# Performance work log

Measured on AMD Instinct MI355X. Metric: run time of the kernel, lower is better.

The kernel has to match this reference:

```python
import jax, jax.numpy as jnp
import numpy as np

B, T, C, E, KB, V = 2, 2048, 128, 16, 32, 50257
EPS = 1e-5


def layernorm(x, g, b):
    mu = jnp.mean(x, axis=-1, keepdims=True)
    var = jnp.mean((x - mu) ** 2, axis=-1, keepdims=True)
    return (x - mu) * jax.lax.rsqrt(var + EPS) * g + b


def setup_inputs() -> dict:
    key = jax.random.key(0)
    ks = jax.random.split(key, 16)
    s = 0.02
    return {
        "input_ids": jax.random.randint(ks[0], (B, T), 0, V),
        "emb": jax.random.normal(ks[1], (V, C), jnp.float32) * s,
        "router": jax.random.normal(ks[2], (E, C), jnp.float32) * s,
        "k_experts": jax.random.normal(ks[3], (E, KB, C), jnp.float32),
        "v_experts": jax.random.normal(ks[4], (E, KB, C), jnp.float32),
        "static_k": jax.random.normal(ks[5], (1, 1, KB, C), jnp.float32),
        "static_v": jax.random.normal(ks[6], (1, 1, KB, C), jnp.float32),
        "kv_gate": jnp.float32(0.0),
        "Wq": jax.random.normal(ks[7], (C, C), jnp.float32) * s,
        "Wo": jax.random.normal(ks[8], (C, C), jnp.float32) * s,
        "Wmlp": jax.random.normal(ks[9], (C, C), jnp.float32) * s,
        "bmlp": jnp.zeros((C,), jnp.float32),
        "ln1_g": jnp.ones((C,), jnp.float32),
        "ln1_b": jnp.zeros((C,), jnp.float32),
        "ln2_g": jnp.ones((C,), jnp.float32),
        "ln2_b": jnp.zeros((C,), jnp.float32),
        "Wlm": jax.random.normal(ks[10], (V, C), jnp.float32) * s,
    }


def reference(input_ids, emb, router, k_experts, v_experts, static_k, static_v,
              kv_gate, Wq, Wo, Wmlp, bmlp, ln1_g, ln1_b, ln2_g, ln2_b, Wlm):
    x = emb[input_ids]                                   # [B,T,C]
    x_ln = layernorm(x, ln1_g, ln1_b)
    # routing: dense softmax over E experts per token
    gate_logits = jnp.einsum('btc,ec->bte', x_ln, router)
    rw = jax.nn.softmax(gate_logits, axis=-1)
    dyn_k = jnp.einsum('bte,ekc->btkc', rw, k_experts)   # [B,T,KB,C]
    dyn_v = jnp.einsum('bte,ekc->btkc', rw, v_experts)
    g = jax.nn.sigmoid(kv_gate)
    k_final = g * dyn_k + (1 - g) * static_k             # broadcast [1,1,KB,C]
    v_final = g * dyn_v + (1 - g) * static_v
    # per-token 1-query / KB-key SDPA with scale 1/sqrt(C)
    q = jnp.einsum('btc,dc->btd', x_ln, Wq)
    scores = jnp.einsum('btc,btkc->btk', q, k_final) / jnp.sqrt(jnp.float32(C))
    attn = jax.nn.softmax(scores, axis=-1)
    attn_out = jnp.einsum('btk,btkc->btc', attn, v_final)
    attn_out = jnp.einsum('btc,dc->btd', attn_out, Wo)
    x = x + attn_out
    x = x + jnp.einsum('btc,dc->btd', layernorm(x, ln2_g, ln2_b), Wmlp) + bmlp
    logits = jnp.einsum('btc,vc->btv', x, Wlm)
    return logits, gate_logits
```

## Files before the change

### kernel.cpp

```cpp
#include <hip/hip_runtime.h>
#include <hip/hip_bf16.h>

#define CC   128
#define EE   16
#define KBB  32
#define VV   50257
#define BT   4096

typedef __bf16 bf16x8 __attribute__((ext_vector_type(8)));
typedef float  f32x4  __attribute__((ext_vector_type(4)));

__device__ inline unsigned short f2b(float f) {
    unsigned int i = __builtin_bit_cast(unsigned int, f);
    unsigned int r = (i + 0x7fffu + ((i >> 16) & 1u)) >> 16;
    return (unsigned short)r;
}

__device__ inline float dotf(const float* __restrict__ p,
                             const float* __restrict__ sx) {
    float acc = 0.f;
#pragma unroll
    for (int c = 0; c < CC; c += 4) {
        const float4 a = *reinterpret_cast<const float4*>(p + c);
        const float4 b = *reinterpret_cast<const float4*>(sx + c);
        acc += a.x * b.x + a.y * b.y + a.z * b.z + a.w * b.w;
    }
    return acc;
}

__device__ inline float wsum(float v) {
#pragma unroll
    for (int m = 1; m < 64; m <<= 1) v += __shfl_xor(v, m, 64);
    return v;
}

__device__ inline float bsum128(float v, float* s_red) {
    v = wsum(v);
    __syncthreads();
    if ((threadIdx.x & 63) == 0) s_red[threadIdx.x >> 6] = v;
    __syncthreads();
    return s_red[0] + s_red[1];
}

__global__ __launch_bounds__(128)
void token_kernel(const int* __restrict__ ids,
                  const float* __restrict__ emb,
                  const float* __restrict__ router,
                  const float* __restrict__ k_ex,
                  const float* __restrict__ v_ex,
                  const float* __restrict__ st_k,
                  const float* __restrict__ st_v,
                  const float* __restrict__ kv_gate,
                  const float* __restrict__ Wq,
                  const float* __restrict__ Wo,
                  const float* __restrict__ Wmlp,
                  const float* __restrict__ bmlp,
                  const float* __restrict__ g1,
                  const float* __restrict__ b1,
                  const float* __restrict__ g2,
                  const float* __restrict__ b2v,
                  float* __restrict__ gate_out,
                  unsigned short* __restrict__ xf_out)
{
    __shared__ __align__(16) float s_xln[CC];
    __shared__ __align__(16) float s_q[CC];
    __shared__ __align__(16) float s_m[EE * KBB];
    __shared__ __align__(16) float s_w[EE * KBB];
    __shared__ __align__(16) float s_pa[2 * CC];
    __shared__ __align__(16) float s_ao[CC];
    __shared__ __align__(16) float s_y[CC];
    __shared__ float s_ge[EE], s_rw[EE], s_sc[KBB], s_at[KBB], s_red[2];

    const int tid = threadIdx.x;
    const int t = blockIdx.x;

    const int id = ids[t];
    const float x0 = emb[(size_t)id * CC + tid];

    const float mu = bsum128(x0, s_red) * (1.f / CC);
    const float dx = x0 - mu;
    const float var = bsum128(dx * dx, s_red) * (1.f / CC);
    const float xln = dx * rsqrtf(var + 1e-5f) * g1[tid] + b1[tid];
    s_xln[tid] = xln;
    __syncthreads();

    if (tid < EE) {
        const float acc = dotf(router + tid * CC, s_xln);
        s_ge[tid] = acc;
        gate_out[(size_t)t * EE + tid] = acc;
    }
    __syncthreads();
    float gm = s_ge[0];
#pragma unroll
    for (int e = 1; e < EE; e++) gm = fmaxf(gm, s_ge[e]);
    float gs = 0.f;
#pragma unroll
    for (int e = 0; e < EE; e++) gs += expf(s_ge[e] - gm);
    if (tid < EE) s_rw[tid] = expf(s_ge[tid] - gm) / gs;
    const float gg = 1.f / (1.f + expf(-kv_gate[0]));

    s_q[tid] = dotf(Wq + tid * CC, s_xln);
    __syncthreads();

    for (int r = tid; r < EE * KBB; r += 128)
        s_m[r] = dotf(k_ex + (size_t)r * CC, s_q);
    __syncthreads();

    if (tid < KBB) {
        float accs = 0.f;
#pragma unroll
        for (int e = 0; e < EE; e++) accs += s_rw[e] * s_m[e * KBB + tid];
        const float accst = dotf(st_k + tid * CC, s_q);
        s_sc[tid] = (gg * accs + (1.f - gg) * accst) * 0.08838834764831845f;
    }
    __syncthreads();
    float am = s_sc[0];
#pragma unroll
    for (int k = 1; k < KBB; k++) am = fmaxf(am, s_sc[k]);
    float as = 0.f;
#pragma unroll
    for (int k = 0; k < KBB; k++) as += expf(s_sc[k] - am);
    if (tid < KBB) s_at[tid] = expf(s_sc[tid] - am) / as;
    __syncthreads();

    for (int r = tid; r < EE * KBB; r += 128) s_w[r] = s_rw[r >> 5] * s_at[r & 31];
    __syncthreads();

    {
        const int h = tid >> 6;
        const int c0 = (tid & 63) * 2;
        const int rbase = h * 256;
        float a0 = 0.f, a1 = 0.f;
#pragma unroll 4
        for (int r = 0; r < 256; r++) {
            const float2 u =
                *reinterpret_cast<const float2*>(v_ex + (size_t)(rbase + r) * CC + c0);
            const float wgt = s_w[rbase + r];
            a0 += wgt * u.x;
            a1 += wgt * u.y;
        }
        s_pa[h * CC + c0] = a0;
        s_pa[h * CC + c0 + 1] = a1;
    }
    __syncthreads();

    {
        float stat = 0.f;
#pragma unroll
        for (int k = 0; k < KBB; k++) stat += s_at[k] * st_v[k * CC + tid];
        s_ao[tid] = gg * (s_pa[tid] + s_pa[CC + tid]) + (1.f - gg) * stat;
    }
    __syncthreads();

    const float xr = x0 + dotf(Wo + tid * CC, s_ao);

    const float mu2 = bsum128(xr, s_red) * (1.f / CC);
    const float dx2 = xr - mu2;
    const float var2 = bsum128(dx2 * dx2, s_red) * (1.f / CC);
    s_y[tid] = dx2 * rsqrtf(var2 + 1e-5f) * g2[tid] + b2v[tid];
    __syncthreads();

    const float xf = xr + dotf(Wmlp + tid * CC, s_y) + bmlp[tid];
    xf_out[(size_t)t * CC + tid] = f2b(xf);
}

__global__ __launch_bounds__(256)
void convert_kernel(const float* __restrict__ src,
                    unsigned short* __restrict__ dst, int n8)
{
    const int i = blockIdx.x * 256 + threadIdx.x;
    if (i >= n8) return;
    const float4 a = *reinterpret_cast<const float4*>(src + (size_t)i * 8);
    const float4 b = *reinterpret_cast<const float4*>(src + (size_t)i * 8 + 4);
    unsigned short v[8] = {f2b(a.x), f2b(a.y), f2b(a.z), f2b(a.w),
                           f2b(b.x), f2b(b.y), f2b(b.z), f2b(b.w)};
    *reinterpret_cast<uint4*>(dst + (size_t)i * 8) = *reinterpret_cast<uint4*>(v);
}

__global__ __launch_bounds__(256)
void lm_kernel(const unsigned short* __restrict__ xf,
               const unsigned short* __restrict__ wlm,
               float* __restrict__ out)
{
    const int lane = threadIdx.x & 63;
    const int wid  = threadIdx.x >> 6;
    const int nl   = lane & 15;
    const int quad = lane >> 4;
    const int t0 = blockIdx.x * 64;
    const int v0 = blockIdx.y * 256 + wid * 64;

    bf16x8 a[4][4];
    const unsigned short* abase = xf + (size_t)(t0 + nl) * CC + quad * 8;
#pragma unroll
    for (int mi = 0; mi < 4; mi++)
#pragma unroll
        for (int ks = 0; ks < 4; ks++)
            a[mi][ks] = *reinterpret_cast<const bf16x8*>(abase + (size_t)mi * 16 * CC + ks * 32);

    f32x4 acc[4][4];
#pragma unroll
    for (int mi = 0; mi < 4; mi++)
#pragma unroll
        for (int ni = 0; ni < 4; ni++)
            acc[mi][ni] = (f32x4){0.f, 0.f, 0.f, 0.f};

#pragma unroll
    for (int ni = 0; ni < 4; ni++) {
        const int vr = v0 + ni * 16 + nl;
        const int vrc = vr < VV ? vr : VV - 1;
        const unsigned short* bbase = wlm + (size_t)vrc * CC + quad * 8;
        bf16x8 b[4];
#pragma unroll
        for (int ks = 0; ks < 4; ks++)
            b[ks] = *reinterpret_cast<const bf16x8*>(bbase + ks * 32);
#pragma unroll
        for (int mi = 0; mi < 4; mi++)
#pragma unroll
            for (int ks = 0; ks < 4; ks++)
                acc[mi][ni] = __builtin_amdgcn_mfma_f32_16x16x32_bf16(a[mi][ks], b[ks],
                                                                      acc[mi][ni], 0, 0, 0);
    }

#pragma unroll
    for (int ni = 0; ni < 4; ni++) {
        const int col = v0 + ni * 16 + nl;
        if (col < VV) {
#pragma unroll
            for (int mi = 0; mi < 4; mi++) {
                const size_t rowb = (size_t)(t0 + mi * 16 + quad * 4) * VV + col;
#pragma unroll
                for (int r = 0; r < 4; r++)
                    out[rowb + (size_t)r * VV] = acc[mi][ni][r];
            }
        }
    }
}

extern "C" void kernel_launch(void* const* d_in, const int* in_sizes, int n_in,
                              void* d_out, int out_size, void* d_ws, size_t ws_size,
                              hipStream_t stream)
{
    const int*   ids    = (const int*)d_in[0];
    const float* emb    = (const float*)d_in[1];
    const float* router = (const float*)d_in[2];
    const float* k_ex   = (const float*)d_in[3];
    const float* v_ex   = (const float*)d_in[4];
    const float* st_k   = (const float*)d_in[5];
    const float* st_v   = (const float*)d_in[6];
    const float* kvg    = (const float*)d_in[7];
    const float* Wq     = (const float*)d_in[8];
    const float* Wo     = (const float*)d_in[9];
    const float* Wmlp   = (const float*)d_in[10];
    const float* bmlp   = (const float*)d_in[11];
    const float* g1     = (const float*)d_in[12];
    const float* b1     = (const float*)d_in[13];
    const float* g2     = (const float*)d_in[14];
    const float* b2v    = (const float*)d_in[15];
    const float* wlm    = (const float*)d_in[16];

    float* out      = (float*)d_out;
    float* gate_out = out + (size_t)BT * VV;

    unsigned short* xfbuf = (unsigned short*)d_ws;
    unsigned short* wlmb  = xfbuf + (size_t)BT * CC;

    token_kernel<<<dim3(BT), dim3(128), 0, stream>>>(
        ids, emb, router, k_ex, v_ex, st_k, st_v, kvg,
        Wq, Wo, Wmlp, bmlp, g1, b1, g2, b2v, gate_out, xfbuf);

    const int n8 = (VV * CC) / 8;
    convert_kernel<<<dim3((n8 + 255) / 256), dim3(256), 0, stream>>>(wlm, wlmb, n8);

    lm_kernel<<<dim3(64, 197), dim3(256), 0, stream>>>(xfbuf, wlmb, out);
}
```

Baseline: 1.419 ms.

## Batch eight tokens per block in token kernel to reuse weight loads

The per-token kernel now processes eight tokens per 256-thread block, so every weight row (Wq, expert keys/values, Wo, Wmlp) is loaded once and applied to several tokens held in shared memory. The block-level reductions are replaced by warp shuffles within 32-lane groups. This is meant to cut redundant global and L2 weight traffic and the many barriers in the token stage. In exchange the block uses much more shared memory and launches fewer blocks, and the token stage is probably small next to the LM-head GEMM.

```diff
diff --git a/kernel.cpp b/kernel.cpp
--- a/kernel.cpp
+++ b/kernel.cpp
@@ -6,6 +6,7 @@
 #define KBB  32
 #define VV   50257
 #define BT   4096
+#define TB   8
 
 typedef __bf16 bf16x8 __attribute__((ext_vector_type(8)));
 typedef float  f32x4  __attribute__((ext_vector_type(4)));
@@ -16,33 +17,11 @@
     return (unsigned short)r;
 }
 
-__device__ inline float dotf(const float* __restrict__ p,
-                             const float* __restrict__ sx) {
-    float acc = 0.f;
-#pragma unroll
-    for (int c = 0; c < CC; c += 4) {
-        const float4 a = *reinterpret_cast<const float4*>(p + c);
-        const float4 b = *reinterpret_cast<const float4*>(sx + c);
-        acc += a.x * b.x + a.y * b.y + a.z * b.z + a.w * b.w;
-    }
-    return acc;
-}
-
-__device__ inline float wsum(float v) {
-#pragma unroll
-    for (int m = 1; m < 64; m <<= 1) v += __shfl_xor(v, m, 64);
-    return v;
-}
-
-__device__ inline float bsum128(float v, float* s_red) {
-    v = wsum(v);
-    __syncthreads();
-    if ((threadIdx.x & 63) == 0) s_red[threadIdx.x >> 6] = v;
-    __syncthreads();
-    return s_red[0] + s_red[1];
-}
-
-__global__ __launch_bounds__(128)
+__device__ inline float dot4(const float4 a, const float4 b) {
+    return a.x * b.x + a.y * b.y + a.z * b.z + a.w * b.w;
+}
+
+__global__ __launch_bounds__(256)
 void token_kernel(const int* __restrict__ ids,
                   const float* __restrict__ emb,
                   const float* __restrict__ router,
@@ -62,106 +41,250 @@
                   float* __restrict__ gate_out,
                   unsigned short* __restrict__ xf_out)
 {
-    __shared__ __align__(16) float s_xln[CC];
-    __shared__ __align__(16) float s_q[CC];
-    __shared__ __align__(16) float s_m[EE * KBB];
-    __shared__ __align__(16) float s_w[EE * KBB];
-    __shared__ __align__(16) float s_pa[2 * CC];
-    __shared__ __align__(16) float s_ao[CC];
-    __shared__ __align__(16) float s_y[CC];
-    __shared__ float s_ge[EE], s_rw[EE], s_sc[KBB], s_at[KBB], s_red[2];
+    __shared__ __align__(16) float s_xln[TB][CC];
+    __shared__ __align__(16) float s_x0 [TB][CC];
+    __shared__ __align__(16) float s_q  [TB][CC];
+    __shared__ __align__(16) float s_mw [TB * EE * KBB];
+    __shared__ __align__(16) float s_part[8][TB][CC];
+    __shared__ __align__(16) float s_ao [TB][CC];
+    __shared__ __align__(16) float s_xr [TB][CC];
+    __shared__ float s_rw[TB][EE];
+    __shared__ float s_at[TB][KBB];
 
     const int tid = threadIdx.x;
-    const int t = blockIdx.x;
-
-    const int id = ids[t];
-    const float x0 = emb[(size_t)id * CC + tid];
-
-    const float mu = bsum128(x0, s_red) * (1.f / CC);
-    const float dx = x0 - mu;
-    const float var = bsum128(dx * dx, s_red) * (1.f / CC);
-    const float xln = dx * rsqrtf(var + 1e-5f) * g1[tid] + b1[tid];
-    s_xln[tid] = xln;
-    __syncthreads();
-
-    if (tid < EE) {
-        const float acc = dotf(router + tid * CC, s_xln);
-        s_ge[tid] = acc;
-        gate_out[(size_t)t * EE + tid] = acc;
-    }
-    __syncthreads();
-    float gm = s_ge[0];
-#pragma unroll
-    for (int e = 1; e < EE; e++) gm = fmaxf(gm, s_ge[e]);
-    float gs = 0.f;
-#pragma unroll
-    for (int e = 0; e < EE; e++) gs += expf(s_ge[e] - gm);
-    if (tid < EE) s_rw[tid] = expf(s_ge[tid] - gm) / gs;
+    const int t0g = blockIdx.x * TB;
+
     const float gg = 1.f / (1.f + expf(-kv_gate[0]));
 
-    s_q[tid] = dotf(Wq + tid * CC, s_xln);
-    __syncthreads();
-
-    for (int r = tid; r < EE * KBB; r += 128)
-        s_m[r] = dotf(k_ex + (size_t)r * CC, s_q);
-    __syncthreads();
-
-    if (tid < KBB) {
+    const int tA = tid >> 5;
+    const int cA = (tid & 31) * 4;
+    const int dV = tid & 127;
+    const int tgV = (tid >> 7) * 4;
+
+    {
+        const int id = ids[t0g + tA];
+        const float4 x0 = *reinterpret_cast<const float4*>(emb + (size_t)id * CC + cA);
+        float s = x0.x + x0.y + x0.z + x0.w;
+#pragma unroll
+        for (int mk = 1; mk < 32; mk <<= 1) s += __shfl_xor(s, mk, 64);
+        const float mu = s * (1.f / CC);
+        float4 d;
+        d.x = x0.x - mu; d.y = x0.y - mu; d.z = x0.z - mu; d.w = x0.w - mu;
+        float v = d.x * d.x + d.y * d.y + d.z * d.z + d.w * d.w;
+#pragma unroll
+        for (int mk = 1; mk < 32; mk <<= 1) v += __shfl_xor(v, mk, 64);
+        const float rs = rsqrtf(v * (1.f / CC) + 1e-5f);
+        const float4 gv = *reinterpret_cast<const float4*>(g1 + cA);
+        const float4 bv = *reinterpret_cast<const float4*>(b1 + cA);
+        float4 xl;
+        xl.x = d.x * rs * gv.x + bv.x;
+        xl.y = d.y * rs * gv.y + bv.y;
+        xl.z = d.z * rs * gv.z + bv.z;
+        xl.w = d.w * rs * gv.w + bv.w;
+        *reinterpret_cast<float4*>(&s_xln[tA][cA]) = xl;
+        *reinterpret_cast<float4*>(&s_x0[tA][cA]) = x0;
+    }
+    __syncthreads();
+
+    {
+        const int e = tid & 15;
+        const int half = (tid >> 4) & 1;
+        const float* rp = router + e * CC + half * 64;
+        const float* xp = &s_xln[tA][half * 64];
+        float acc = 0.f;
+#pragma unroll
+        for (int c = 0; c < 64; c += 4)
+            acc += dot4(*reinterpret_cast<const float4*>(rp + c),
+                        *reinterpret_cast<const float4*>(xp + c));
+        acc += __shfl_xor(acc, 16, 64);
+        if (half == 0) gate_out[(size_t)(t0g + tA) * EE + e] = acc;
+        float mx = acc;
+#pragma unroll
+        for (int mk = 1; mk < 16; mk <<= 1) mx = fmaxf(mx, __shfl_xor(mx, mk, 64));
+        const float ex = expf(acc - mx);
+        float ss = ex;
+#pragma unroll
+        for (int mk = 1; mk < 16; mk <<= 1) ss += __shfl_xor(ss, mk, 64);
+        if (half == 0) s_rw[tA][e] = ex / ss;
+    }
+
+    {
+        const float* wp = Wq + dV * CC;
+        float a0 = 0.f, a1 = 0.f, a2 = 0.f, a3 = 0.f;
+#pragma unroll 8
+        for (int c = 0; c < CC; c += 4) {
+            const float4 w = *reinterpret_cast<const float4*>(wp + c);
+            a0 += dot4(w, *reinterpret_cast<const float4*>(&s_xln[tgV + 0][c]));
+            a1 += dot4(w, *reinterpret_cast<const float4*>(&s_xln[tgV + 1][c]));
+            a2 += dot4(w, *reinterpret_cast<const float4*>(&s_xln[tgV + 2][c]));
+            a3 += dot4(w, *reinterpret_cast<const float4*>(&s_xln[tgV + 3][c]));
+        }
+        s_q[tgV + 0][dV] = a0;
+        s_q[tgV + 1][dV] = a1;
+        s_q[tgV + 2][dV] = a2;
+        s_q[tgV + 3][dV] = a3;
+    }
+    __syncthreads();
+
+    {
+        const int r0 = tid * 2;
+        const float* k0p = k_ex + (size_t)r0 * CC;
+        const float* k1p = k0p + CC;
+        float acc0[TB] = {0.f, 0.f, 0.f, 0.f, 0.f, 0.f, 0.f, 0.f};
+        float acc1[TB] = {0.f, 0.f, 0.f, 0.f, 0.f, 0.f, 0.f, 0.f};
+#pragma unroll 4
+        for (int c = 0; c < CC; c += 4) {
+            const float4 k0 = *reinterpret_cast<const float4*>(k0p + c);
+            const float4 k1 = *reinterpret_cast<const float4*>(k1p + c);
+#pragma unroll
+            for (int t = 0; t < TB; t++) {
+                const float4 q = *reinterpret_cast<const float4*>(&s_q[t][c]);
+                acc0[t] += dot4(k0, q);
+                acc1[t] += dot4(k1, q);
+            }
+        }
+#pragma unroll
+        for (int t = 0; t < TB; t++) {
+            s_mw[t * (EE * KBB) + r0]     = acc0[t];
+            s_mw[t * (EE * KBB) + r0 + 1] = acc1[t];
+        }
+    }
+    __syncthreads();
+
+    {
+        const int k = tid & 31;
         float accs = 0.f;
 #pragma unroll
-        for (int e = 0; e < EE; e++) accs += s_rw[e] * s_m[e * KBB + tid];
-        const float accst = dotf(st_k + tid * CC, s_q);
-        s_sc[tid] = (gg * accs + (1.f - gg) * accst) * 0.08838834764831845f;
-    }
-    __syncthreads();
-    float am = s_sc[0];
-#pragma unroll
-    for (int k = 1; k < KBB; k++) am = fmaxf(am, s_sc[k]);
-    float as = 0.f;
-#pragma unroll
-    for (int k = 0; k < KBB; k++) as += expf(s_sc[k] - am);
-    if (tid < KBB) s_at[tid] = expf(s_sc[tid] - am) / as;
-    __syncthreads();
-
-    for (int r = tid; r < EE * KBB; r += 128) s_w[r] = s_rw[r >> 5] * s_at[r & 31];
-    __syncthreads();
-
-    {
-        const int h = tid >> 6;
-        const int c0 = (tid & 63) * 2;
-        const int rbase = h * 256;
-        float a0 = 0.f, a1 = 0.f;
-#pragma unroll 4
-        for (int r = 0; r < 256; r++) {
-            const float2 u =
-                *reinterpret_cast<const float2*>(v_ex + (size_t)(rbase + r) * CC + c0);
-            const float wgt = s_w[rbase + r];
-            a0 += wgt * u.x;
-            a1 += wgt * u.y;
-        }
-        s_pa[h * CC + c0] = a0;
-        s_pa[h * CC + c0 + 1] = a1;
-    }
-    __syncthreads();
-
-    {
-        float stat = 0.f;
-#pragma unroll
-        for (int k = 0; k < KBB; k++) stat += s_at[k] * st_v[k * CC + tid];
-        s_ao[tid] = gg * (s_pa[tid] + s_pa[CC + tid]) + (1.f - gg) * stat;
-    }
-    __syncthreads();
-
-    const float xr = x0 + dotf(Wo + tid * CC, s_ao);
-
-    const float mu2 = bsum128(xr, s_red) * (1.f / CC);
-    const float dx2 = xr - mu2;
-    const float var2 = bsum128(dx2 * dx2, s_red) * (1.f / CC);
-    s_y[tid] = dx2 * rsqrtf(var2 + 1e-5f) * g2[tid] + b2v[tid];
-    __syncthreads();
-
-    const float xf = xr + dotf(Wmlp + tid * CC, s_y) + bmlp[tid];
-    xf_out[(size_t)t * CC + tid] = f2b(xf);
+        for (int e = 0; e < EE; e++)
+            accs += s_rw[tA][e] * s_mw[tA * (EE * KBB) + e * KBB + k];
+        const float* kp = st_k + k * CC;
+        float accst = 0.f;
+#pragma unroll 8
+        for (int c = 0; c < CC; c += 4)
+            accst += dot4(*reinterpret_cast<const float4*>(kp + c),
+                          *reinterpret_cast<const float4*>(&s_q[tA][c]));
+        const float sc = (gg * accs + (1.f - gg) * accst) * 0.08838834764831845f;
+        float mx = sc;
+#pragma unroll
+        for (int mk = 1; mk < 32; mk <<= 1) mx = fmaxf(mx, __shfl_xor(mx, mk, 64));
+        const float ex = expf(sc - mx);
+        float ss = ex;
+#pragma unroll
+        for (int mk = 1; mk < 32; mk <<= 1) ss += __shfl_xor(ss, mk, 64);
+        s_at[tA][k] = ex / ss;
+    }
+    __syncthreads();
+
+    {
+#pragma unroll
+        for (int i = 0; i < (TB * EE * KBB) / 256; i++) {
+            const int idx = tid + i * 256;
+            const int r = idx >> 3;
+            const int t = idx & 7;
+            s_mw[r * TB + t] = gg * s_rw[t][r >> 5] * s_at[t][r & 31];
+        }
+    }
+    __syncthreads();
+
+    {
+        const int g = tid >> 5;
+        const int rbase = g * 64;
+        f32x4 acc0 = {0.f, 0.f, 0.f, 0.f}, acc1 = acc0, acc2 = acc0, acc3 = acc0;
+        f32x4 acc4 = acc0, acc5 = acc0, acc6 = acc0, acc7 = acc0;
+#pragma unroll 2
+        for (int r = 0; r < 64; r++) {
+            const f32x4 v = *reinterpret_cast<const f32x4*>(
+                v_ex + (size_t)(rbase + r) * CC + cA);
+            const float4 w0 = *reinterpret_cast<const float4*>(&s_mw[(rbase + r) * TB]);
+            const float4 w1 = *reinterpret_cast<const float4*>(&s_mw[(rbase + r) * TB + 4]);
+            acc0 += w0.x * v; acc1 += w0.y * v; acc2 += w0.z * v; acc3 += w0.w * v;
+            acc4 += w1.x * v; acc5 += w1.y * v; acc6 += w1.z * v; acc7 += w1.w * v;
+        }
+        *reinterpret_cast<f32x4*>(&s_part[g][0][cA]) = acc0;
+        *reinterpret_cast<f32x4*>(&s_part[g][1][cA]) = acc1;
+        *reinterpret_cast<f32x4*>(&s_part[g][2][cA]) = acc2;
+        *reinterpret_cast<f32x4*>(&s_part[g][3][cA]) = acc3;
+        *reinterpret_cast<f32x4*>(&s_part[g][4][cA]) = acc4;
+        *reinterpret_cast<f32x4*>(&s_part[g][5][cA]) = acc5;
+        *reinterpret_cast<f32x4*>(&s_part[g][6][cA]) = acc6;
+        *reinterpret_cast<f32x4*>(&s_part[g][7][cA]) = acc7;
+    }
+    __syncthreads();
+
+    {
+        f32x4 pa = {0.f, 0.f, 0.f, 0.f};
+#pragma unroll
+        for (int g = 0; g < 8; g++)
+            pa += *reinterpret_cast<const f32x4*>(&s_part[g][tA][cA]);
+        f32x4 stat = {0.f, 0.f, 0.f, 0.f};
+#pragma unroll 8
+        for (int k = 0; k < KBB; k++) {
+            const f32x4 sv = *reinterpret_cast<const f32x4*>(st_v + k * CC + cA);
+            stat += s_at[tA][k] * sv;
+        }
+        const f32x4 ao = pa + (1.f - gg) * stat;
+        *reinterpret_cast<f32x4*>(&s_ao[tA][cA]) = ao;
+    }
+    __syncthreads();
+
+    {
+        const float* wp = Wo + dV * CC;
+        float a0 = 0.f, a1 = 0.f, a2 = 0.f, a3 = 0.f;
+#pragma unroll 8
+        for (int c = 0; c < CC; c += 4) {
+            const float4 w = *reinterpret_cast<const float4*>(wp + c);
+            a0 += dot4(w, *reinterpret_cast<const float4*>(&s_ao[tgV + 0][c]));
+            a1 += dot4(w, *reinterpret_cast<const float4*>(&s_ao[tgV + 1][c]));
+            a2 += dot4(w, *reinterpret_cast<const float4*>(&s_ao[tgV + 2][c]));
+            a3 += dot4(w, *reinterpret_cast<const float4*>(&s_ao[tgV + 3][c]));
+        }
+        s_xr[tgV + 0][dV] = s_x0[tgV + 0][dV] + a0;
+        s_xr[tgV + 1][dV] = s_x0[tgV + 1][dV] + a1;
+        s_xr[tgV + 2][dV] = s_x0[tgV + 2][dV] + a2;
+        s_xr[tgV + 3][dV] = s_x0[tgV + 3][dV] + a3;
+    }
+    __syncthreads();
+
+    {
+        const float4 xr = *reinterpret_cast<const float4*>(&s_xr[tA][cA]);
+        float s = xr.x + xr.y + xr.z + xr.w;
+#pragma unroll
+        for (int mk = 1; mk < 32; mk <<= 1) s += __shfl_xor(s, mk, 64);
+        const float mu = s * (1.f / CC);
+        float4 d;
+        d.x = xr.x - mu; d.y = xr.y - mu; d.z = xr.z - mu; d.w = xr.w - mu;
+        float v = d.x * d.x + d.y * d.y + d.z * d.z + d.w * d.w;
+#pragma unroll
+        for (int mk = 1; mk < 32; mk <<= 1) v += __shfl_xor(v, mk, 64);
+        const float rs = rsqrtf(v * (1.f / CC) + 1e-5f);
+        const float4 gv = *reinterpret_cast<const float4*>(g2 + cA);
+        const float4 bv = *reinterpret_cast<const float4*>(b2v + cA);
+        float4 y;
+        y.x = d.x * rs * gv.x + bv.x;
+        y.y = d.y * rs * gv.y + bv.y;
+        y.z = d.z * rs * gv.z + bv.z;
+        y.w = d.w * rs * gv.w + bv.w;
+        *reinterpret_cast<float4*>(&s_ao[tA][cA]) = y;
+    }
+    __syncthreads();
+
+    {
+        const float* wp = Wmlp + dV * CC;
+        float a0 = 0.f, a1 = 0.f, a2 = 0.f, a3 = 0.f;
+#pragma unroll 8
+        for (int c = 0; c < CC; c += 4) {
+            const float4 w = *reinterpret_cast<const float4*>(wp + c);
+            a0 += dot4(w, *reinterpret_cast<const float4*>(&s_ao[tgV + 0][c]));
+            a1 += dot4(w, *reinterpret_cast<const float4*>(&s_ao[tgV + 1][c]));
+            a2 += dot4(w, *reinterpret_cast<const float4*>(&s_ao[tgV + 2][c]));
+            a3 += dot4(w, *reinterpret_cast<const float4*>(&s_ao[tgV + 3][c]));
+        }
+        const float bm = bmlp[dV];
+        xf_out[(size_t)(t0g + tgV + 0) * CC + dV] = f2b(s_xr[tgV + 0][dV] + a0 + bm);
+        xf_out[(size_t)(t0g + tgV + 1) * CC + dV] = f2b(s_xr[tgV + 1][dV] + a1 + bm);
+        xf_out[(size_t)(t0g + tgV + 2) * CC + dV] = f2b(s_xr[tgV + 2][dV] + a2 + bm);
+        xf_out[(size_t)(t0g + tgV + 3) * CC + dV] = f2b(s_xr[tgV + 3][dV] + a3 + bm);
+    }
 }
 
 __global__ __launch_bounds__(256)
@@ -264,7 +387,7 @@
     unsigned short* xfbuf = (unsigned short*)d_ws;
     unsigned short* wlmb  = xfbuf + (size_t)BT * CC;
 
-    token_kernel<<<dim3(BT), dim3(128), 0, stream>>>(
+    token_kernel<<<dim3(BT / TB), dim3(256), 0, stream>>>(
         ids, emb, router, k_ex, v_ex, st_k, st_v, kvg,
         Wq, Wo, Wmlp, bmlp, g1, b1, g2, b2v, gate_out, xfbuf);
 
```

After: 1.189 ms. 1.19x faster.
